# Performance work log

Measured on AMD Instinct MI355X. Metric: run time of the kernel, lower is better.

## Reference

```python
import jax, jax.numpy as jnp
import numpy as np

B, T, D = 2, 1024, 2048      # batch, seq, model dim
E, F, K = 64, 512, 4          # n_experts, expert hidden, top-k
S, HS = 2, 512 * 4            # shared experts, shared hidden = expert_dim * topk


def setup_inputs() -> dict:
    key = jax.random.key(0)
    ks = jax.random.split(key, 9)
    s = 0.02
    f32 = jnp.float32
    return {
        "x": jax.random.normal(ks[0], (B, T, D), f32),
        "router_w": jax.random.normal(ks[1], (D, E), f32) * s,
        "router_bias": jnp.zeros((E,), f32),
        "wg": jax.random.normal(ks[2], (E, D, F), f32) * s,
        "wu": jax.random.normal(ks[3], (E, D, F), f32) * s,
        "wd": jax.random.normal(ks[4], (E, F, D), f32) * s,
        "swg": jax.random.normal(ks[5], (S, D, HS), f32) * s,
        "swu": jax.random.normal(ks[6], (S, D, HS), f32) * s,
        "swd": jax.random.normal(ks[7], (S, HS, D), f32) * s,
    }


def reference(x, router_w, router_bias, wg, wu, wd, swg, swu, swd):
    b, t, d = x.shape
    flat = x.reshape(b * t, d)                      # [N, D]
    n = flat.shape[0]

    # Router: softmax scores, top-k selection on (logits + bias)
    logits = flat @ router_w                         # [N, E]
    scores = jax.nn.softmax(logits, axis=-1)
    _, topk_idx = jax.lax.top_k(logits + router_bias, K)          # [N, K]
    topk_scores = jnp.take_along_axis(scores, topk_idx, axis=-1)  # [N, K]
    topk_scores = topk_scores / topk_scores.sum(axis=-1, keepdims=True)

    # Dense combine weights: w[n, e] = normalized score if expert e selected else 0
    comb = jnp.zeros((n, E), dtype=flat.dtype).at[
        jnp.arange(n)[:, None], topk_idx].set(topk_scores)        # [N, E]

    # Routed experts (SwiGLU), computed densely and masked by combine weights
    g = jax.nn.silu(jnp.einsum('nd,edf->nef', flat, wg))          # [N, E, F]
    u = jnp.einsum('nd,edf->nef', flat, wu)                       # [N, E, F]
    routed = jnp.einsum('ne,nef,efd->nd', comb, g * u, wd)        # [N, D]

    # Shared experts (always active, summed)
    sg = jax.nn.silu(jnp.einsum('nd,sdh->nsh', flat, swg))        # [N, S, HS]
    su = jnp.einsum('nd,sdh->nsh', flat, swu)
    shared = jnp.einsum('nsh,shd->nd', sg * su, swd)              # [N, D]

    return (routed + shared).reshape(b, t, d)
```

## Files before the change

kernel.cpp:

```cpp
#include <hip/hip_runtime.h>
#include <hip/hip_bf16.h>

typedef __bf16 bf16x8 __attribute__((ext_vector_type(8)));
typedef float f32x4 __attribute__((ext_vector_type(4)));
typedef unsigned short u16x4 __attribute__((ext_vector_type(4)));
typedef unsigned short u16x8 __attribute__((ext_vector_type(8)));

#define DEVI __device__ __forceinline__

constexpr int N_TOK = 2048;
constexpr int DIM   = 2048;
constexpr int NEXP  = 64;
constexpr int FDIM  = 512;
constexpr int TOPK  = 4;
constexpr int NSH   = 2;
constexpr int HSH   = 2048;

constexpr int BK = 64, KS = 8;

DEVI unsigned short f2b(float f) {
  union { float fv; unsigned u; } v; v.fv = f;
  unsigned r = v.u + 0x7fffu + ((v.u >> 16) & 1u);
  return (unsigned short)(r >> 16);
}
DEVI float b2f(unsigned short h) {
  union { unsigned u; float f; } v; v.u = ((unsigned)h) << 16;
  return v.f;
}
DEVI void gll16(const void* g, void* l) {
  __builtin_amdgcn_global_load_lds((const __attribute__((address_space(1))) unsigned*)g,
                                   (__attribute__((address_space(3))) unsigned*)l, 16, 0, 0);
}

__global__ void cvt_x_kernel(const float* __restrict__ x, unsigned short* __restrict__ xb) {
  const size_t i = ((size_t)blockIdx.x * 256 + threadIdx.x) * 8;
  const float4 a = *reinterpret_cast<const float4*>(x + i);
  const float4 b = *reinterpret_cast<const float4*>(x + i + 4);
  u16x8 o;
  o[0] = f2b(a.x); o[1] = f2b(a.y); o[2] = f2b(a.z); o[3] = f2b(a.w);
  o[4] = f2b(b.x); o[5] = f2b(b.y); o[6] = f2b(b.z); o[7] = f2b(b.w);
  *reinterpret_cast<u16x8*>(xb + i) = o;
}

__global__ __launch_bounds__(256)
void tr_shared_kernel(const float* __restrict__ swu, const float* __restrict__ swg,
                      const float* __restrict__ swd, unsigned short* __restrict__ swuT,
                      unsigned short* __restrict__ swgT, unsigned short* __restrict__ swdT) {
  __shared__ float Lf[64][68];
  const int tid = threadIdx.x;
  const int r0 = blockIdx.x * 64, c0 = blockIdx.y * 64;
  const int z = blockIdx.z, mat = z >> 1;
  const size_t soff = (size_t)(z & 1) * DIM * HSH;
  const float* in = (mat == 0 ? swu : mat == 1 ? swg : swd) + soff;
  unsigned short* ot = (mat == 0 ? swuT : mat == 1 ? swgT : swdT) + soff;
  #pragma unroll
  for (int j = 0; j < 4; ++j) {
    const int idx = j * 1024 + tid * 4;
    const int row = idx >> 6, col = idx & 63;
    const float4 v = *reinterpret_cast<const float4*>(in + (size_t)(r0 + row) * 2048 + c0 + col);
    *reinterpret_cast<float4*>(&Lf[row][col]) = v;
  }
  __syncthreads();
  #pragma unroll
  for (int j = 0; j < 4; ++j) {
    const int idx = j * 1024 + tid * 4;
    const int orow = idx >> 6, ocol = idx & 63;
    u16x4 o;
    o[0] = f2b(Lf[ocol][orow]);     o[1] = f2b(Lf[ocol + 1][orow]);
    o[2] = f2b(Lf[ocol + 2][orow]); o[3] = f2b(Lf[ocol + 3][orow]);
    *reinterpret_cast<u16x4*>(ot + (size_t)(c0 + orow) * 2048 + r0 + ocol) = o;
  }
}

__global__ __launch_bounds__(256)
void router_kernel(const float* __restrict__ x, const float* __restrict__ rw,
                   const float* __restrict__ rb, int* __restrict__ cnt,
                   int* __restrict__ listTok, float* __restrict__ listW) {
  __shared__ float Lx[8][128];
  const int tid = threadIdx.x;
  const int lane = tid & 63;
  const int wave = tid >> 6;
  const int tokBase = blockIdx.x * 8;

  float acc0 = 0.f, acc1 = 0.f;
  for (int dc = 0; dc < DIM; dc += 128) {
    __syncthreads();
    {
      const int idx = tid * 4;
      const int row = idx >> 7, col = idx & 127;
      *reinterpret_cast<float4*>(&Lx[row][col]) =
          *reinterpret_cast<const float4*>(x + (size_t)(tokBase + row) * DIM + dc + col);
    }
    __syncthreads();
    #pragma unroll 16
    for (int dd = 0; dd < 128; ++dd) {
      const float r = rw[(size_t)(dc + dd) * NEXP + lane];
      acc0 = fmaf(Lx[wave * 2 + 0][dd], r, acc0);
      acc1 = fmaf(Lx[wave * 2 + 1][dd], r, acc1);
    }
  }

  const float bias = rb[lane];
  #pragma unroll
  for (int t = 0; t < 2; ++t) {
    const float v = (t == 0) ? acc0 : acc1;
    const int token = tokBase + wave * 2 + t;
    float m = v;
    #pragma unroll
    for (int o = 32; o > 0; o >>= 1) m = fmaxf(m, __shfl_xor(m, o));
    const float p = expf(v - m);
    float ss = p;
    #pragma unroll
    for (int o = 32; o > 0; o >>= 1) ss += __shfl_xor(ss, o);
    const float score = p / ss;
    float cur = v + bias;
    float wk[TOPK]; int ik[TOPK]; float wsum = 0.f;
    #pragma unroll
    for (int k = 0; k < TOPK; ++k) {
      float tm = cur;
      #pragma unroll
      for (int o = 32; o > 0; o >>= 1) tm = fmaxf(tm, __shfl_xor(tm, o));
      const unsigned long long msk = __ballot(cur == tm);
      const int sel = (int)__builtin_ctzll(msk);
      const float w = __shfl(score, sel);
      wk[k] = w; ik[k] = sel; wsum += w;
      if (lane == sel) cur = -3.4e38f;
    }
    if (lane < TOPK) {
      const int e = ik[lane];
      const float w = wk[lane] / wsum;
      const int slot = atomicAdd(&cnt[e], 1);
      listTok[(size_t)e * N_TOK + slot] = token;
      listW[(size_t)e * N_TOK + slot] = w;
    }
  }
}

__global__ void scan_kernel(const int* __restrict__ cnt, int* __restrict__ off) {
  if (threadIdx.x == 0) {
    int s = 0;
    for (int e = 0; e < NEXP; ++e) { off[e] = s; s += cnt[e]; }
  }
}

template<bool GPASS>
__global__ __launch_bounds__(256, 2)
void up_routed(const unsigned short* __restrict__ xb, const float* __restrict__ W,
               const int* __restrict__ cnt, const int* __restrict__ off,
               const int* __restrict__ listTok, const float* __restrict__ listW,
               unsigned short* __restrict__ H) {
  const int tid = threadIdx.x;
  const int f0 = blockIdx.x * 128;
  const int e  = blockIdx.y;
  const int m0 = blockIdx.z * 128;
  const int c = cnt[e];
  if (m0 >= c) return;
  const int rcnt = min(128, c - m0);
  const int rowbase = off[e] + m0;

  __shared__ __align__(16) unsigned short Al[KS][128][8];
  __shared__ __align__(16) unsigned short Bl[KS][128][8];
  __shared__ int tokS[128];
  __shared__ float wS[128];

  if (tid < 128) {
    tokS[tid] = listTok[(size_t)e * N_TOK + m0 + min(tid, rcnt - 1)];
    wS[tid] = (tid < rcnt) ? listW[(size_t)e * N_TOK + m0 + tid] : 0.f;
  }
  __syncthreads();

  const int wid = tid >> 6, l = tid & 63;
  const int wm = wid >> 1, wn = wid & 1;
  const int lc = l & 15, hi = l >> 4;

  const unsigned short* pa0 = xb + (size_t)tokS[l] * DIM;
  const unsigned short* pa1 = xb + (size_t)tokS[64 + l] * DIM;
  const float* bw = W + (size_t)e * DIM * FDIM + f0;
  const int f4 = tid & 31, k4a = tid >> 5;

  f32x4 acc[4][4];
  #pragma unroll
  for (int i = 0; i < 4; ++i)
    #pragma unroll
    for (int j = 0; j < 4; ++j) acc[i][j] = f32x4{0.f, 0.f, 0.f, 0.f};

  for (int d0 = 0; d0 < DIM; d0 += BK) {
    gll16(pa0 + d0 + (2 * wid) * 8,     &Al[2 * wid][0][0]);
    gll16(pa1 + d0 + (2 * wid) * 8,     &Al[2 * wid][64][0]);
    gll16(pa0 + d0 + (2 * wid + 1) * 8, &Al[2 * wid + 1][0][0]);
    gll16(pa1 + d0 + (2 * wid + 1) * 8, &Al[2 * wid + 1][64][0]);
    f32x4 rB[2][4];
    #pragma unroll
    for (int s2 = 0; s2 < 2; ++s2)
      #pragma unroll
      for (int j = 0; j < 4; ++j)
        rB[s2][j] = *reinterpret_cast<const f32x4*>(
            bw + (size_t)(d0 + k4a * 8 + s2 * 4 + j) * FDIM + f4 * 4);
    #pragma unroll
    for (int cc = 0; cc < 4; ++cc) {
      u16x8 v;
      v[0] = f2b(rB[0][0][cc]); v[1] = f2b(rB[0][1][cc]);
      v[2] = f2b(rB[0][2][cc]); v[3] = f2b(rB[0][3][cc]);
      v[4] = f2b(rB[1][0][cc]); v[5] = f2b(rB[1][1][cc]);
      v[6] = f2b(rB[1][2][cc]); v[7] = f2b(rB[1][3][cc]);
      *reinterpret_cast<u16x8*>(&Bl[k4a][f4 * 4 + cc][0]) = v;
    }
    __syncthreads();
    #pragma unroll
    for (int ks = 0; ks < 2; ++ks) {
      bf16x8 af[4], bq[4];
      #pragma unroll
      for (int i = 0; i < 4; ++i)
        af[i] = *reinterpret_cast<const bf16x8*>(&Al[ks * 4 + hi][wm * 64 + i * 16 + lc][0]);
      #pragma unroll
      for (int i = 0; i < 4; ++i)
        bq[i] = *reinterpret_cast<const bf16x8*>(&Bl[ks * 4 + hi][wn * 64 + i * 16 + lc][0]);
      #pragma unroll
      for (int mi = 0; mi < 4; ++mi)
        #pragma unroll
        for (int ni = 0; ni < 4; ++ni)
          acc[mi][ni] = __builtin_amdgcn_mfma_f32_16x16x32_bf16(af[mi], bq[ni], acc[mi][ni], 0, 0, 0);
    }
    __syncthreads();
  }

  #pragma unroll
  for (int mi = 0; mi < 4; ++mi)
    #pragma unroll
    for (int ni = 0; ni < 4; ++ni)
      #pragma unroll
      for (int r2 = 0; r2 < 4; ++r2) {
        const int row = wm * 64 + mi * 16 + hi * 4 + r2;
        if (row < rcnt) {
          const int col = f0 + wn * 64 + ni * 16 + lc;
          const size_t idx = (size_t)(rowbase + row) * FDIM + col;
          const float v = acc[mi][ni][r2];
          if constexpr (GPASS) {
            const float u = b2f(H[idx]);
            H[idx] = f2b((v / (1.f + __expf(-v))) * u * wS[row]);
          } else {
            H[idx] = f2b(v);
          }
        }
      }
}

__global__ __launch_bounds__(256, 2)
void up_shared(const unsigned short* __restrict__ xb,
               const unsigned short* __restrict__ WuT, const unsigned short* __restrict__ WgT,
               unsigned short* __restrict__ H) {
  const int tid = threadIdx.x;
  const int f0 = blockIdx.x * 64;
  const int s  = blockIdx.y;
  const int m0 = blockIdx.z * 128;

  __shared__ __align__(16) unsigned short Al[KS][128][8];
  __shared__ __align__(16) unsigned short Bu[KS][64][8];
  __shared__ __align__(16) unsigned short Bg[KS][64][8];

  const int wid = tid >> 6, l = tid & 63;
  const int wm = wid >> 1, wn = wid & 1;
  const int lc = l & 15, hi = l >> 4;

  const unsigned short* pa0 = xb + (size_t)(m0 + l) * DIM;
  const unsigned short* pa1 = xb + (size_t)(m0 + 64 + l) * DIM;
  const unsigned short* pbu = WuT + (size_t)s * HSH * DIM + (size_t)(f0 + l) * DIM;
  const unsigned short* pbg = WgT + (size_t)s * HSH * DIM + (size_t)(f0 + l) * DIM;

  f32x4 aU[4][2], aG[4][2];
  #pragma unroll
  for (int i = 0; i < 4; ++i)
    #pragma unroll
    for (int j = 0; j < 2; ++j) { aU[i][j] = f32x4{0.f,0.f,0.f,0.f}; aG[i][j] = f32x4{0.f,0.f,0.f,0.f}; }

  for (int d0 = 0; d0 < DIM; d0 += BK) {
    gll16(pa0 + d0 + (2 * wid) * 8,     &Al[2 * wid][0][0]);
    gll16(pa1 + d0 + (2 * wid) * 8,     &Al[2 * wid][64][0]);
    gll16(pa0 + d0 + (2 * wid + 1) * 8, &Al[2 * wid + 1][0][0]);
    gll16(pa1 + d0 + (2 * wid + 1) * 8, &Al[2 * wid + 1][64][0]);
    gll16(pbu + d0 + (2 * wid) * 8,     &Bu[2 * wid][0][0]);
    gll16(pbu + d0 + (2 * wid + 1) * 8, &Bu[2 * wid + 1][0][0]);
    gll16(pbg + d0 + (2 * wid) * 8,     &Bg[2 * wid][0][0]);
    gll16(pbg + d0 + (2 * wid + 1) * 8, &Bg[2 * wid + 1][0][0]);
    __syncthreads();
    #pragma unroll
    for (int ks = 0; ks < 2; ++ks) {
      bf16x8 af[4], bu[2], bg[2];
      #pragma unroll
      for (int i = 0; i < 4; ++i)
        af[i] = *reinterpret_cast<const bf16x8*>(&Al[ks * 4 + hi][wm * 64 + i * 16 + lc][0]);
      #pragma unroll
      for (int i = 0; i < 2; ++i) {
        bu[i] = *reinterpret_cast<const bf16x8*>(&Bu[ks * 4 + hi][wn * 32 + i * 16 + lc][0]);
        bg[i] = *reinterpret_cast<const bf16x8*>(&Bg[ks * 4 + hi][wn * 32 + i * 16 + lc][0]);
      }
      #pragma unroll
      for (int mi = 0; mi < 4; ++mi)
        #pragma unroll
        for (int ni = 0; ni < 2; ++ni) {
          aU[mi][ni] = __builtin_amdgcn_mfma_f32_16x16x32_bf16(af[mi], bu[ni], aU[mi][ni], 0, 0, 0);
          aG[mi][ni] = __builtin_amdgcn_mfma_f32_16x16x32_bf16(af[mi], bg[ni], aG[mi][ni], 0, 0, 0);
        }
    }
    __syncthreads();
  }

  #pragma unroll
  for (int mi = 0; mi < 4; ++mi)
    #pragma unroll
    for (int ni = 0; ni < 2; ++ni)
      #pragma unroll
      for (int r2 = 0; r2 < 4; ++r2) {
        const int row = wm * 64 + mi * 16 + hi * 4 + r2;
        const int col = f0 + wn * 32 + ni * 16 + lc;
        const float g = aG[mi][ni][r2], u = aU[mi][ni][r2];
        const float h = (g / (1.f + __expf(-g))) * u;
        H[((size_t)s * N_TOK + m0 + row) * HSH + col] = f2b(h);
      }
}

__global__ __launch_bounds__(256, 2)
void down_all(const unsigned short* __restrict__ Hr, const unsigned short* __restrict__ Hs,
              const float* __restrict__ wd, const unsigned short* __restrict__ swdT,
              const int* __restrict__ cnt, const int* __restrict__ off,
              const int* __restrict__ listTok, float* __restrict__ out) {
  const int tid = threadIdx.x;
  const int x0 = blockIdx.x * 128;
  const int y  = blockIdx.y;
  const int m0 = blockIdx.z * 128;
  const bool routed = y < NEXP;

  __shared__ __align__(16) unsigned short Al[KS][128][8];
  __shared__ __align__(16) unsigned short Bl[KS][128][8];
  __shared__ int tokS[128];

  const int wid = tid >> 6, l = tid & 63;
  const int wm = wid >> 1, wn = wid & 1;
  const int lc = l & 15, hi = l >> 4;

  int rcnt = 128, Kd;
  const unsigned short *pa0, *pa1, *pb0 = nullptr, *pb1 = nullptr;
  const float* bw = nullptr;

  if (routed) {
    const int c = cnt[y];
    if (m0 >= c) return;
    rcnt = min(128, c - m0);
    const int rowbase = off[y] + m0;
    Kd = FDIM;
    if (tid < 128) tokS[tid] = listTok[(size_t)y * N_TOK + m0 + min(tid, rcnt - 1)];
    pa0 = Hr + (size_t)(rowbase + min(l, rcnt - 1)) * FDIM;
    pa1 = Hr + (size_t)(rowbase + min(64 + l, rcnt - 1)) * FDIM;
    bw = wd + (size_t)y * FDIM * DIM + x0;
  } else {
    const int s = y - NEXP;
    Kd = HSH;
    if (tid < 128) tokS[tid] = m0 + tid;
    pa0 = Hs + ((size_t)s * N_TOK + m0 + l) * HSH;
    pa1 = Hs + ((size_t)s * N_TOK + m0 + 64 + l) * HSH;
    pb0 = swdT + (size_t)s * HSH * DIM + (size_t)(x0 + l) * HSH;
    pb1 = swdT + (size_t)s * HSH * DIM + (size_t)(x0 + 64 + l) * HSH;
  }

  const int f4 = tid & 31, k4a = tid >> 5;

  f32x4 acc[4][4];
  #pragma unroll
  for (int i = 0; i < 4; ++i)
    #pragma unroll
    for (int j = 0; j < 4; ++j) acc[i][j] = f32x4{0.f, 0.f, 0.f, 0.f};

  for (int d0 = 0; d0 < Kd; d0 += BK) {
    gll16(pa0 + d0 + (2 * wid) * 8,     &Al[2 * wid][0][0]);
    gll16(pa1 + d0 + (2 * wid) * 8,     &Al[2 * wid][64][0]);
    gll16(pa0 + d0 + (2 * wid + 1) * 8, &Al[2 * wid + 1][0][0]);
    gll16(pa1 + d0 + (2 * wid + 1) * 8, &Al[2 * wid + 1][64][0]);
    if (routed) {
      f32x4 rB[2][4];
      #pragma unroll
      for (int s2 = 0; s2 < 2; ++s2)
        #pragma unroll
        for (int j = 0; j < 4; ++j)
          rB[s2][j] = *reinterpret_cast<const f32x4*>(
              bw + (size_t)(d0 + k4a * 8 + s2 * 4 + j) * DIM + f4 * 4);
      #pragma unroll
      for (int cc = 0; cc < 4; ++cc) {
        u16x8 v;
        v[0] = f2b(rB[0][0][cc]); v[1] = f2b(rB[0][1][cc]);
        v[2] = f2b(rB[0][2][cc]); v[3] = f2b(rB[0][3][cc]);
        v[4] = f2b(rB[1][0][cc]); v[5] = f2b(rB[1][1][cc]);
        v[6] = f2b(rB[1][2][cc]); v[7] = f2b(rB[1][3][cc]);
        *reinterpret_cast<u16x8*>(&Bl[k4a][f4 * 4 + cc][0]) = v;
      }
    } else {
      gll16(pb0 + d0 + (2 * wid) * 8,     &Bl[2 * wid][0][0]);
      gll16(pb1 + d0 + (2 * wid) * 8,     &Bl[2 * wid][64][0]);
      gll16(pb0 + d0 + (2 * wid + 1) * 8, &Bl[2 * wid + 1][0][0]);
      gll16(pb1 + d0 + (2 * wid + 1) * 8, &Bl[2 * wid + 1][64][0]);
    }
    __syncthreads();
    #pragma unroll
    for (int ks = 0; ks < 2; ++ks) {
      bf16x8 af[4], bq[4];
      #pragma unroll
      for (int i = 0; i < 4; ++i)
        af[i] = *reinterpret_cast<const bf16x8*>(&Al[ks * 4 + hi][wm * 64 + i * 16 + lc][0]);
      #pragma unroll
      for (int i = 0; i < 4; ++i)
        bq[i] = *reinterpret_cast<const bf16x8*>(&Bl[ks * 4 + hi][wn * 64 + i * 16 + lc][0]);
      #pragma unroll
      for (int mi = 0; mi < 4; ++mi)
        #pragma unroll
        for (int ni = 0; ni < 4; ++ni)
          acc[mi][ni] = __builtin_amdgcn_mfma_f32_16x16x32_bf16(af[mi], bq[ni], acc[mi][ni], 0, 0, 0);
    }
    __syncthreads();
  }

  #pragma unroll
  for (int mi = 0; mi < 4; ++mi)
    #pragma unroll
    for (int ni = 0; ni < 4; ++ni)
      #pragma unroll
      for (int r2 = 0; r2 < 4; ++r2) {
        const int row = wm * 64 + mi * 16 + hi * 4 + r2;
        if (row < rcnt) {
          const int col = x0 + wn * 64 + ni * 16 + lc;
          atomicAdd(&out[(size_t)tokS[row] * DIM + col], acc[mi][ni][r2]);
        }
      }
}

extern "C" void kernel_launch(void* const* d_in, const int* in_sizes, int n_in,
                              void* d_out, int out_size, void* d_ws, size_t ws_size,
                              hipStream_t stream) {
  const float* x   = (const float*)d_in[0];
  const float* rw  = (const float*)d_in[1];
  const float* rb  = (const float*)d_in[2];
  const float* wg  = (const float*)d_in[3];
  const float* wu  = (const float*)d_in[4];
  const float* wd  = (const float*)d_in[5];
  const float* swg = (const float*)d_in[6];
  const float* swu = (const float*)d_in[7];
  const float* swd = (const float*)d_in[8];
  float* out = (float*)d_out;
  char* ws = (char*)d_ws;

  int* cnt = (int*)ws;
  int* off = (int*)(ws + 256);
  int* listTok = (int*)(ws + 4096);
  float* listW = (float*)(ws + 4096 + 512 * 1024);
  unsigned short* xb   = (unsigned short*)(ws + (size_t) 2 * 1024 * 1024);
  unsigned short* Hr   = (unsigned short*)(ws + (size_t)10 * 1024 * 1024);
  unsigned short* Hs   = (unsigned short*)(ws + (size_t)18 * 1024 * 1024);
  unsigned short* swuT = (unsigned short*)(ws + (size_t)34 * 1024 * 1024);
  unsigned short* swgT = (unsigned short*)(ws + (size_t)50 * 1024 * 1024);
  unsigned short* swdT = (unsigned short*)(ws + (size_t)66 * 1024 * 1024);

  hipMemsetAsync(cnt, 0, NEXP * sizeof(int), stream);
  hipMemsetAsync(out, 0, (size_t)N_TOK * DIM * sizeof(float), stream);
  cvt_x_kernel<<<(N_TOK * DIM) / (256 * 8), 256, 0, stream>>>(x, xb);
  tr_shared_kernel<<<dim3(32, 32, 6), 256, 0, stream>>>(swu, swg, swd, swuT, swgT, swdT);
  router_kernel<<<N_TOK / 8, 256, 0, stream>>>(x, rw, rb, cnt, listTok, listW);
  scan_kernel<<<1, 64, 0, stream>>>(cnt, off);

  up_routed<false><<<dim3(FDIM / 128, NEXP, 16), 256, 0, stream>>>(
      xb, wu, cnt, off, listTok, listW, Hr);
  up_routed<true><<<dim3(FDIM / 128, NEXP, 16), 256, 0, stream>>>(
      xb, wg, cnt, off, listTok, listW, Hr);
  up_shared<<<dim3(HSH / 64, NSH, N_TOK / 128), 256, 0, stream>>>(
      xb, swuT, swgT, Hs);
  down_all<<<dim3(DIM / 128, NEXP + NSH, 16), 256, 0, stream>>>(
      Hr, Hs, wd, swdT, cnt, off, listTok, out);
}
```

Measured before the change: 687.6 us.

## Fuse routed gate/up GEMMs, double-buffer pipelines, replace atomic scatter with combine

The separate up and gate passes over routed experts become one kernel that computes both accumulators and applies SwiGLU in the epilogue, so the gathered activations are read once. All GEMM kernels move to double-buffered LDS with explicit vmcnt waits, so the next tile's loads overlap the current MFMAs. The down projection splits into a shared kernel that writes out directly (the memset goes away) and a routed kernel that writes bf16 partials. A combine kernel then sums each token's four partials, replacing float atomics. This adds a partials buffer, an extra launch and bf16 rounding of the partials.

```diff
diff --git a/kernel.cpp b/kernel.cpp
--- a/kernel.cpp
+++ b/kernel.cpp
@@ -17,6 +17,12 @@
 constexpr int HSH   = 2048;
 
 constexpr int BK = 64, KS = 8;
+
+#define WAIT_VM0 asm volatile("s_waitcnt vmcnt(0)" ::: "memory")
+#define WAIT_VM8 asm volatile("s_waitcnt vmcnt(8)" ::: "memory")
+#define WAIT_LG0 asm volatile("s_waitcnt lgkmcnt(0)" ::: "memory")
+#define SBAR __builtin_amdgcn_s_barrier()
+#define SCHED0 __builtin_amdgcn_sched_barrier(0)
 
 DEVI unsigned short f2b(float f) {
   union { float fv; unsigned u; } v; v.fv = f;
@@ -75,7 +81,8 @@
 __global__ __launch_bounds__(256)
 void router_kernel(const float* __restrict__ x, const float* __restrict__ rw,
                    const float* __restrict__ rb, int* __restrict__ cnt,
-                   int* __restrict__ listTok, float* __restrict__ listW) {
+                   int* __restrict__ listTok, float* __restrict__ listW,
+                   int* __restrict__ tokEP) {
   __shared__ float Lx[8][128];
   const int tid = threadIdx.x;
   const int lane = tid & 63;
@@ -132,6 +139,7 @@
       const int slot = atomicAdd(&cnt[e], 1);
       listTok[(size_t)e * N_TOK + slot] = token;
       listW[(size_t)e * N_TOK + slot] = w;
+      tokEP[token * TOPK + lane] = (e << 16) | slot;
     }
   }
 }
@@ -143,14 +151,15 @@
   }
 }
 
-template<bool GPASS>
 __global__ __launch_bounds__(256, 2)
-void up_routed(const unsigned short* __restrict__ xb, const float* __restrict__ W,
+void up_routed(const unsigned short* __restrict__ xb,
+               const float* __restrict__ Wu, const float* __restrict__ Wg,
                const int* __restrict__ cnt, const int* __restrict__ off,
                const int* __restrict__ listTok, const float* __restrict__ listW,
                unsigned short* __restrict__ H) {
+  constexpr int NT = DIM / BK;
   const int tid = threadIdx.x;
-  const int f0 = blockIdx.x * 128;
+  const int f0 = blockIdx.x * 64;
   const int e  = blockIdx.y;
   const int m0 = blockIdx.z * 128;
   const int c = cnt[e];
@@ -158,44 +167,316 @@
   const int rcnt = min(128, c - m0);
   const int rowbase = off[e] + m0;
 
-  __shared__ __align__(16) unsigned short Al[KS][128][8];
-  __shared__ __align__(16) unsigned short Bl[KS][128][8];
-  __shared__ int tokS[128];
-  __shared__ float wS[128];
-
-  if (tid < 128) {
-    tokS[tid] = listTok[(size_t)e * N_TOK + m0 + min(tid, rcnt - 1)];
-    wS[tid] = (tid < rcnt) ? listW[(size_t)e * N_TOK + m0 + tid] : 0.f;
-  }
+  __shared__ __align__(16) unsigned short Al[2][KS][128][8];
+  __shared__ __align__(16) unsigned short BuL[2][KS][64][8];
+  __shared__ __align__(16) unsigned short BgL[2][KS][64][8];
+  __shared__ float wSs[128];
+
+  if (tid < 128) wSs[tid] = (tid < rcnt) ? listW[(size_t)e * N_TOK + m0 + tid] : 0.f;
   __syncthreads();
 
   const int wid = tid >> 6, l = tid & 63;
   const int wm = wid >> 1, wn = wid & 1;
   const int lc = l & 15, hi = l >> 4;
 
-  const unsigned short* pa0 = xb + (size_t)tokS[l] * DIM;
-  const unsigned short* pa1 = xb + (size_t)tokS[64 + l] * DIM;
-  const float* bw = W + (size_t)e * DIM * FDIM + f0;
-  const int f4 = tid & 31, k4a = tid >> 5;
-
-  f32x4 acc[4][4];
+  const int t0 = listTok[(size_t)e * N_TOK + m0 + min(l, rcnt - 1)];
+  const int t1 = listTok[(size_t)e * N_TOK + m0 + min(64 + l, rcnt - 1)];
+  const unsigned short* pa0 = xb + (size_t)t0 * DIM;
+  const unsigned short* pa1 = xb + (size_t)t1 * DIM;
+  const float* wub = Wu + (size_t)e * DIM * FDIM + f0;
+  const float* wgb = Wg + (size_t)e * DIM * FDIM + f0;
+
+  const int q = tid & 31, p = tid >> 5;
+  const int c4 = (q & 15) * 4, kh = q >> 4;
+
+  f32x4 rBu[4], rBg[4];
+  auto loadB = [&](int g) {
+    const int d0 = g * BK;
+    #pragma unroll
+    for (int j = 0; j < 4; ++j)
+      rBu[j] = *reinterpret_cast<const f32x4*>(wub + (size_t)(d0 + p * 8 + kh * 4 + j) * FDIM + c4);
+    #pragma unroll
+    for (int j = 0; j < 4; ++j)
+      rBg[j] = *reinterpret_cast<const f32x4*>(wgb + (size_t)(d0 + p * 8 + kh * 4 + j) * FDIM + c4);
+  };
+  auto stageA = [&](int g, int b) {
+    const int d0 = g * BK;
+    gll16(pa0 + d0 + (2 * wid) * 8,     &Al[b][2 * wid][0][0]);
+    gll16(pa1 + d0 + (2 * wid) * 8,     &Al[b][2 * wid][64][0]);
+    gll16(pa0 + d0 + (2 * wid + 1) * 8, &Al[b][2 * wid + 1][0][0]);
+    gll16(pa1 + d0 + (2 * wid + 1) * 8, &Al[b][2 * wid + 1][64][0]);
+  };
+  auto writeB = [&](int b) {
+    #pragma unroll
+    for (int cc = 0; cc < 4; ++cc) {
+      u16x4 vu, vg;
+      #pragma unroll
+      for (int j = 0; j < 4; ++j) { vu[j] = f2b(rBu[j][cc]); vg[j] = f2b(rBg[j][cc]); }
+      *reinterpret_cast<u16x4*>(&BuL[b][p][c4 + cc][kh * 4]) = vu;
+      *reinterpret_cast<u16x4*>(&BgL[b][p][c4 + cc][kh * 4]) = vg;
+    }
+  };
+
+  f32x4 aU[4][2], aG[4][2];
   #pragma unroll
   for (int i = 0; i < 4; ++i)
     #pragma unroll
-    for (int j = 0; j < 4; ++j) acc[i][j] = f32x4{0.f, 0.f, 0.f, 0.f};
-
-  for (int d0 = 0; d0 < DIM; d0 += BK) {
-    gll16(pa0 + d0 + (2 * wid) * 8,     &Al[2 * wid][0][0]);
-    gll16(pa1 + d0 + (2 * wid) * 8,     &Al[2 * wid][64][0]);
-    gll16(pa0 + d0 + (2 * wid + 1) * 8, &Al[2 * wid + 1][0][0]);
-    gll16(pa1 + d0 + (2 * wid + 1) * 8, &Al[2 * wid + 1][64][0]);
-    f32x4 rB[2][4];
+    for (int j = 0; j < 2; ++j) { aU[i][j] = f32x4{0,0,0,0}; aG[i][j] = f32x4{0,0,0,0}; }
+
+  loadB(0);
+  stageA(0, 0);
+  SCHED0;
+  writeB(0);
+  loadB(1);
+  WAIT_VM8; WAIT_LG0; SBAR;
+
+  for (int g = 0; g < NT; ++g) {
+    const int b = g & 1;
+    if (g + 1 < NT) {
+      stageA(g + 1, b ^ 1);
+      SCHED0;
+      writeB(b ^ 1);
+      if (g + 2 < NT) loadB(g + 2);
+    }
+    #pragma unroll
+    for (int ks = 0; ks < 2; ++ks) {
+      bf16x8 af[4], bu[2], bg[2];
+      #pragma unroll
+      for (int i = 0; i < 4; ++i)
+        af[i] = *reinterpret_cast<const bf16x8*>(&Al[b][ks * 4 + hi][wm * 64 + i * 16 + lc][0]);
+      #pragma unroll
+      for (int i = 0; i < 2; ++i) {
+        bu[i] = *reinterpret_cast<const bf16x8*>(&BuL[b][ks * 4 + hi][wn * 32 + i * 16 + lc][0]);
+        bg[i] = *reinterpret_cast<const bf16x8*>(&BgL[b][ks * 4 + hi][wn * 32 + i * 16 + lc][0]);
+      }
+      #pragma unroll
+      for (int mi = 0; mi < 4; ++mi)
+        #pragma unroll
+        for (int ni = 0; ni < 2; ++ni) {
+          aU[mi][ni] = __builtin_amdgcn_mfma_f32_16x16x32_bf16(af[mi], bu[ni], aU[mi][ni], 0, 0, 0);
+          aG[mi][ni] = __builtin_amdgcn_mfma_f32_16x16x32_bf16(af[mi], bg[ni], aG[mi][ni], 0, 0, 0);
+        }
+    }
+    if (g + 1 < NT) {
+      if (g + 2 < NT) { WAIT_VM8; } else { WAIT_VM0; }
+      WAIT_LG0; SBAR;
+    }
+  }
+
+  #pragma unroll
+  for (int mi = 0; mi < 4; ++mi)
+    #pragma unroll
+    for (int ni = 0; ni < 2; ++ni)
+      #pragma unroll
+      for (int r2 = 0; r2 < 4; ++r2) {
+        const int row = wm * 64 + mi * 16 + hi * 4 + r2;
+        if (row < rcnt) {
+          const int col = f0 + wn * 32 + ni * 16 + lc;
+          const float g = aG[mi][ni][r2], u = aU[mi][ni][r2];
+          const float h = (g / (1.f + __expf(-g))) * u * wSs[row];
+          H[(size_t)(rowbase + row) * FDIM + col] = f2b(h);
+        }
+      }
+}
+
+__global__ __launch_bounds__(256, 2)
+void up_shared(const unsigned short* __restrict__ xb,
+               const unsigned short* __restrict__ WuT, const unsigned short* __restrict__ WgT,
+               unsigned short* __restrict__ H) {
+  constexpr int NT = DIM / BK;
+  const int tid = threadIdx.x;
+  const int f0 = blockIdx.x * 64;
+  const int s  = blockIdx.y;
+  const int m0 = blockIdx.z * 128;
+
+  __shared__ __align__(16) unsigned short Al[2][KS][128][8];
+  __shared__ __align__(16) unsigned short Bu[2][KS][64][8];
+  __shared__ __align__(16) unsigned short Bg[2][KS][64][8];
+
+  const int wid = tid >> 6, l = tid & 63;
+  const int wm = wid >> 1, wn = wid & 1;
+  const int lc = l & 15, hi = l >> 4;
+
+  const unsigned short* pa0 = xb + (size_t)(m0 + l) * DIM;
+  const unsigned short* pa1 = xb + (size_t)(m0 + 64 + l) * DIM;
+  const unsigned short* pbu = WuT + (size_t)s * HSH * DIM + (size_t)(f0 + l) * DIM;
+  const unsigned short* pbg = WgT + (size_t)s * HSH * DIM + (size_t)(f0 + l) * DIM;
+
+  auto stage = [&](int g, int b) {
+    const int d0 = g * BK;
+    gll16(pa0 + d0 + (2 * wid) * 8,     &Al[b][2 * wid][0][0]);
+    gll16(pa1 + d0 + (2 * wid) * 8,     &Al[b][2 * wid][64][0]);
+    gll16(pa0 + d0 + (2 * wid + 1) * 8, &Al[b][2 * wid + 1][0][0]);
+    gll16(pa1 + d0 + (2 * wid + 1) * 8, &Al[b][2 * wid + 1][64][0]);
+    gll16(pbu + d0 + (2 * wid) * 8,     &Bu[b][2 * wid][0][0]);
+    gll16(pbu + d0 + (2 * wid + 1) * 8, &Bu[b][2 * wid + 1][0][0]);
+    gll16(pbg + d0 + (2 * wid) * 8,     &Bg[b][2 * wid][0][0]);
+    gll16(pbg + d0 + (2 * wid + 1) * 8, &Bg[b][2 * wid + 1][0][0]);
+  };
+
+  f32x4 aU[4][2], aG[4][2];
+  #pragma unroll
+  for (int i = 0; i < 4; ++i)
+    #pragma unroll
+    for (int j = 0; j < 2; ++j) { aU[i][j] = f32x4{0,0,0,0}; aG[i][j] = f32x4{0,0,0,0}; }
+
+  stage(0, 0);
+  WAIT_VM0; SBAR;
+
+  for (int g = 0; g < NT; ++g) {
+    const int b = g & 1;
+    if (g + 1 < NT) stage(g + 1, b ^ 1);
+    #pragma unroll
+    for (int ks = 0; ks < 2; ++ks) {
+      bf16x8 af[4], bu[2], bg[2];
+      #pragma unroll
+      for (int i = 0; i < 4; ++i)
+        af[i] = *reinterpret_cast<const bf16x8*>(&Al[b][ks * 4 + hi][wm * 64 + i * 16 + lc][0]);
+      #pragma unroll
+      for (int i = 0; i < 2; ++i) {
+        bu[i] = *reinterpret_cast<const bf16x8*>(&Bu[b][ks * 4 + hi][wn * 32 + i * 16 + lc][0]);
+        bg[i] = *reinterpret_cast<const bf16x8*>(&Bg[b][ks * 4 + hi][wn * 32 + i * 16 + lc][0]);
+      }
+      #pragma unroll
+      for (int mi = 0; mi < 4; ++mi)
+        #pragma unroll
+        for (int ni = 0; ni < 2; ++ni) {
+          aU[mi][ni] = __builtin_amdgcn_mfma_f32_16x16x32_bf16(af[mi], bu[ni], aU[mi][ni], 0, 0, 0);
+          aG[mi][ni] = __builtin_amdgcn_mfma_f32_16x16x32_bf16(af[mi], bg[ni], aG[mi][ni], 0, 0, 0);
+        }
+    }
+    if (g + 1 < NT) { WAIT_VM0; SBAR; }
+  }
+
+  #pragma unroll
+  for (int mi = 0; mi < 4; ++mi)
+    #pragma unroll
+    for (int ni = 0; ni < 2; ++ni)
+      #pragma unroll
+      for (int r2 = 0; r2 < 4; ++r2) {
+        const int row = wm * 64 + mi * 16 + hi * 4 + r2;
+        const int col = f0 + wn * 32 + ni * 16 + lc;
+        const float g = aG[mi][ni][r2], u = aU[mi][ni][r2];
+        H[((size_t)s * N_TOK + m0 + row) * HSH + col] = f2b((g / (1.f + __expf(-g))) * u);
+      }
+}
+
+__global__ __launch_bounds__(256, 3)
+void down_shared(const unsigned short* __restrict__ Hs, const unsigned short* __restrict__ swdT,
+                 float* __restrict__ out) {
+  constexpr int NT = 2 * HSH / BK;
+  const int tid = threadIdx.x;
+  const int x0 = blockIdx.x * 128;
+  const int m0 = blockIdx.z * 64;
+
+  __shared__ __align__(16) unsigned short Al[2][KS][64][8];
+  __shared__ __align__(16) unsigned short Bl[2][KS][128][8];
+
+  const int wid = tid >> 6, l = tid & 63;
+  const int wm = wid >> 1, wn = wid & 1;
+  const int lc = l & 15, hi = l >> 4;
+
+  auto stage = [&](int g, int b) {
+    const int seg = g >> 5;
+    const int d0 = (g & 31) * BK;
+    const unsigned short* sA = Hs + ((size_t)seg * N_TOK + m0 + l) * HSH + d0;
+    const unsigned short* b0 = swdT + (size_t)seg * HSH * DIM + (size_t)(x0 + l) * HSH + d0;
+    const unsigned short* b1 = b0 + (size_t)64 * HSH;
+    gll16(sA + (2 * wid) * 8,     &Al[b][2 * wid][0][0]);
+    gll16(sA + (2 * wid + 1) * 8, &Al[b][2 * wid + 1][0][0]);
+    gll16(b0 + (2 * wid) * 8,     &Bl[b][2 * wid][0][0]);
+    gll16(b1 + (2 * wid) * 8,     &Bl[b][2 * wid][64][0]);
+    gll16(b0 + (2 * wid + 1) * 8, &Bl[b][2 * wid + 1][0][0]);
+    gll16(b1 + (2 * wid + 1) * 8, &Bl[b][2 * wid + 1][64][0]);
+  };
+
+  f32x4 acc[2][4];
+  #pragma unroll
+  for (int i = 0; i < 2; ++i)
+    #pragma unroll
+    for (int j = 0; j < 4; ++j) acc[i][j] = f32x4{0,0,0,0};
+
+  stage(0, 0);
+  WAIT_VM0; SBAR;
+
+  for (int g = 0; g < NT; ++g) {
+    const int b = g & 1;
+    if (g + 1 < NT) stage(g + 1, b ^ 1);
+    #pragma unroll
+    for (int ks = 0; ks < 2; ++ks) {
+      bf16x8 af[2], bq[4];
+      #pragma unroll
+      for (int i = 0; i < 2; ++i)
+        af[i] = *reinterpret_cast<const bf16x8*>(&Al[b][ks * 4 + hi][wm * 32 + i * 16 + lc][0]);
+      #pragma unroll
+      for (int i = 0; i < 4; ++i)
+        bq[i] = *reinterpret_cast<const bf16x8*>(&Bl[b][ks * 4 + hi][wn * 64 + i * 16 + lc][0]);
+      #pragma unroll
+      for (int mi = 0; mi < 2; ++mi)
+        #pragma unroll
+        for (int ni = 0; ni < 4; ++ni)
+          acc[mi][ni] = __builtin_amdgcn_mfma_f32_16x16x32_bf16(af[mi], bq[ni], acc[mi][ni], 0, 0, 0);
+    }
+    if (g + 1 < NT) { WAIT_VM0; SBAR; }
+  }
+
+  #pragma unroll
+  for (int mi = 0; mi < 2; ++mi)
+    #pragma unroll
+    for (int ni = 0; ni < 4; ++ni)
+      #pragma unroll
+      for (int r2 = 0; r2 < 4; ++r2) {
+        const int row = wm * 32 + mi * 16 + hi * 4 + r2;
+        const int col = x0 + wn * 64 + ni * 16 + lc;
+        out[(size_t)(m0 + row) * DIM + col] = acc[mi][ni][r2];
+      }
+}
+
+__global__ __launch_bounds__(256, 2)
+void down_routed(const unsigned short* __restrict__ Hr, const float* __restrict__ wd,
+                 const int* __restrict__ cnt, const int* __restrict__ off,
+                 unsigned short* __restrict__ P) {
+  constexpr int NT = FDIM / BK;
+  const int tid = threadIdx.x;
+  const int x0 = blockIdx.x * 128;
+  const int e  = blockIdx.y;
+  const int m0 = blockIdx.z * 128;
+  const int c = cnt[e];
+  if (m0 >= c) return;
+  const int rcnt = min(128, c - m0);
+  const int rowbase = off[e] + m0;
+
+  __shared__ __align__(16) unsigned short Al[2][KS][128][8];
+  __shared__ __align__(16) unsigned short Bl[2][KS][128][8];
+
+  const int wid = tid >> 6, l = tid & 63;
+  const int wm = wid >> 1, wn = wid & 1;
+  const int lc = l & 15, hi = l >> 4;
+
+  const unsigned short* pa0 = Hr + (size_t)(rowbase + min(l, rcnt - 1)) * FDIM;
+  const unsigned short* pa1 = Hr + (size_t)(rowbase + min(64 + l, rcnt - 1)) * FDIM;
+  const float* bw = wd + (size_t)e * FDIM * DIM + x0;
+
+  const int f4 = tid & 31, p = tid >> 5;
+  const int c4 = f4 * 4;
+
+  f32x4 rB[2][4];
+  auto loadB = [&](int g) {
+    const int d0 = g * BK;
     #pragma unroll
     for (int s2 = 0; s2 < 2; ++s2)
       #pragma unroll
       for (int j = 0; j < 4; ++j)
-        rB[s2][j] = *reinterpret_cast<const f32x4*>(
-            bw + (size_t)(d0 + k4a * 8 + s2 * 4 + j) * FDIM + f4 * 4);
+        rB[s2][j] = *reinterpret_cast<const f32x4*>(bw + (size_t)(d0 + p * 8 + s2 * 4 + j) * DIM + c4);
+  };
+  auto stageA = [&](int g, int b) {
+    const int d0 = g * BK;
+    gll16(pa0 + d0 + (2 * wid) * 8,     &Al[b][2 * wid][0][0]);
+    gll16(pa1 + d0 + (2 * wid) * 8,     &Al[b][2 * wid][64][0]);
+    gll16(pa0 + d0 + (2 * wid + 1) * 8, &Al[b][2 * wid + 1][0][0]);
+    gll16(pa1 + d0 + (2 * wid + 1) * 8, &Al[b][2 * wid + 1][64][0]);
+  };
+  auto writeB = [&](int b) {
     #pragma unroll
     for (int cc = 0; cc < 4; ++cc) {
       u16x8 v;
@@ -203,218 +484,50 @@
       v[2] = f2b(rB[0][2][cc]); v[3] = f2b(rB[0][3][cc]);
       v[4] = f2b(rB[1][0][cc]); v[5] = f2b(rB[1][1][cc]);
       v[6] = f2b(rB[1][2][cc]); v[7] = f2b(rB[1][3][cc]);
-      *reinterpret_cast<u16x8*>(&Bl[k4a][f4 * 4 + cc][0]) = v;
-    }
-    __syncthreads();
+      *reinterpret_cast<u16x8*>(&Bl[b][p][c4 + cc][0]) = v;
+    }
+  };
+
+  f32x4 acc[4][4];
+  #pragma unroll
+  for (int i = 0; i < 4; ++i)
+    #pragma unroll
+    for (int j = 0; j < 4; ++j) acc[i][j] = f32x4{0,0,0,0};
+
+  loadB(0);
+  stageA(0, 0);
+  SCHED0;
+  writeB(0);
+  loadB(1);
+  WAIT_VM8; WAIT_LG0; SBAR;
+
+  for (int g = 0; g < NT; ++g) {
+    const int b = g & 1;
+    if (g + 1 < NT) {
+      stageA(g + 1, b ^ 1);
+      SCHED0;
+      writeB(b ^ 1);
+      if (g + 2 < NT) loadB(g + 2);
+    }
     #pragma unroll
     for (int ks = 0; ks < 2; ++ks) {
       bf16x8 af[4], bq[4];
       #pragma unroll
       for (int i = 0; i < 4; ++i)
-        af[i] = *reinterpret_cast<const bf16x8*>(&Al[ks * 4 + hi][wm * 64 + i * 16 + lc][0]);
+        af[i] = *reinterpret_cast<const bf16x8*>(&Al[b][ks * 4 + hi][wm * 64 + i * 16 + lc][0]);
       #pragma unroll
       for (int i = 0; i < 4; ++i)
-        bq[i] = *reinterpret_cast<const bf16x8*>(&Bl[ks * 4 + hi][wn * 64 + i * 16 + lc][0]);
+        bq[i] = *reinterpret_cast<const bf16x8*>(&Bl[b][ks * 4 + hi][wn * 64 + i * 16 + lc][0]);
       #pragma unroll
       for (int mi = 0; mi < 4; ++mi)
         #pragma unroll
         for (int ni = 0; ni < 4; ++ni)
           acc[mi][ni] = __builtin_amdgcn_mfma_f32_16x16x32_bf16(af[mi], bq[ni], acc[mi][ni], 0, 0, 0);
     }
-    __syncthreads();
-  }
-
-  #pragma unroll
-  for (int mi = 0; mi < 4; ++mi)
-    #pragma unroll
-    for (int ni = 0; ni < 4; ++ni)
-      #pragma unroll
-      for (int r2 = 0; r2 < 4; ++r2) {
-        const int row = wm * 64 + mi * 16 + hi * 4 + r2;
-        if (row < rcnt) {
-          const int col = f0 + wn * 64 + ni * 16 + lc;
-          const size_t idx = (size_t)(rowbase + row) * FDIM + col;
-          const float v = acc[mi][ni][r2];
-          if constexpr (GPASS) {
-            const float u = b2f(H[idx]);
-            H[idx] = f2b((v / (1.f + __expf(-v))) * u * wS[row]);
-          } else {
-            H[idx] = f2b(v);
-          }
-        }
-      }
-}
-
-__global__ __launch_bounds__(256, 2)
-void up_shared(const unsigned short* __restrict__ xb,
-               const unsigned short* __restrict__ WuT, const unsigned short* __restrict__ WgT,
-               unsigned short* __restrict__ H) {
-  const int tid = threadIdx.x;
-  const int f0 = blockIdx.x * 64;
-  const int s  = blockIdx.y;
-  const int m0 = blockIdx.z * 128;
-
-  __shared__ __align__(16) unsigned short Al[KS][128][8];
-  __shared__ __align__(16) unsigned short Bu[KS][64][8];
-  __shared__ __align__(16) unsigned short Bg[KS][64][8];
-
-  const int wid = tid >> 6, l = tid & 63;
-  const int wm = wid >> 1, wn = wid & 1;
-  const int lc = l & 15, hi = l >> 4;
-
-  const unsigned short* pa0 = xb + (size_t)(m0 + l) * DIM;
-  const unsigned short* pa1 = xb + (size_t)(m0 + 64 + l) * DIM;
-  const unsigned short* pbu = WuT + (size_t)s * HSH * DIM + (size_t)(f0 + l) * DIM;
-  const unsigned short* pbg = WgT + (size_t)s * HSH * DIM + (size_t)(f0 + l) * DIM;
-
-  f32x4 aU[4][2], aG[4][2];
-  #pragma unroll
-  for (int i = 0; i < 4; ++i)
-    #pragma unroll
-    for (int j = 0; j < 2; ++j) { aU[i][j] = f32x4{0.f,0.f,0.f,0.f}; aG[i][j] = f32x4{0.f,0.f,0.f,0.f}; }
-
-  for (int d0 = 0; d0 < DIM; d0 += BK) {
-    gll16(pa0 + d0 + (2 * wid) * 8,     &Al[2 * wid][0][0]);
-    gll16(pa1 + d0 + (2 * wid) * 8,     &Al[2 * wid][64][0]);
-    gll16(pa0 + d0 + (2 * wid + 1) * 8, &Al[2 * wid + 1][0][0]);
-    gll16(pa1 + d0 + (2 * wid + 1) * 8, &Al[2 * wid + 1][64][0]);
-    gll16(pbu + d0 + (2 * wid) * 8,     &Bu[2 * wid][0][0]);
-    gll16(pbu + d0 + (2 * wid + 1) * 8, &Bu[2 * wid + 1][0][0]);
-    gll16(pbg + d0 + (2 * wid) * 8,     &Bg[2 * wid][0][0]);
-    gll16(pbg + d0 + (2 * wid + 1) * 8, &Bg[2 * wid + 1][0][0]);
-    __syncthreads();
-    #pragma unroll
-    for (int ks = 0; ks < 2; ++ks) {
-      bf16x8 af[4], bu[2], bg[2];
-      #pragma unroll
-      for (int i = 0; i < 4; ++i)
-        af[i] = *reinterpret_cast<const bf16x8*>(&Al[ks * 4 + hi][wm * 64 + i * 16 + lc][0]);
-      #pragma unroll
-      for (int i = 0; i < 2; ++i) {
-        bu[i] = *reinterpret_cast<const bf16x8*>(&Bu[ks * 4 + hi][wn * 32 + i * 16 + lc][0]);
-        bg[i] = *reinterpret_cast<const bf16x8*>(&Bg[ks * 4 + hi][wn * 32 + i * 16 + lc][0]);
-      }
-      #pragma unroll
-      for (int mi = 0; mi < 4; ++mi)
-        #pragma unroll
-        for (int ni = 0; ni < 2; ++ni) {
-          aU[mi][ni] = __builtin_amdgcn_mfma_f32_16x16x32_bf16(af[mi], bu[ni], aU[mi][ni], 0, 0, 0);
-          aG[mi][ni] = __builtin_amdgcn_mfma_f32_16x16x32_bf16(af[mi], bg[ni], aG[mi][ni], 0, 0, 0);
-        }
-    }
-    __syncthreads();
-  }
-
-  #pragma unroll
-  for (int mi = 0; mi < 4; ++mi)
-    #pragma unroll
-    for (int ni = 0; ni < 2; ++ni)
-      #pragma unroll
-      for (int r2 = 0; r2 < 4; ++r2) {
-        const int row = wm * 64 + mi * 16 + hi * 4 + r2;
-        const int col = f0 + wn * 32 + ni * 16 + lc;
-        const float g = aG[mi][ni][r2], u = aU[mi][ni][r2];
-        const float h = (g / (1.f + __expf(-g))) * u;
-        H[((size_t)s * N_TOK + m0 + row) * HSH + col] = f2b(h);
-      }
-}
-
-__global__ __launch_bounds__(256, 2)
-void down_all(const unsigned short* __restrict__ Hr, const unsigned short* __restrict__ Hs,
-              const float* __restrict__ wd, const unsigned short* __restrict__ swdT,
-              const int* __restrict__ cnt, const int* __restrict__ off,
-              const int* __restrict__ listTok, float* __restrict__ out) {
-  const int tid = threadIdx.x;
-  const int x0 = blockIdx.x * 128;
-  const int y  = blockIdx.y;
-  const int m0 = blockIdx.z * 128;
-  const bool routed = y < NEXP;
-
-  __shared__ __align__(16) unsigned short Al[KS][128][8];
-  __shared__ __align__(16) unsigned short Bl[KS][128][8];
-  __shared__ int tokS[128];
-
-  const int wid = tid >> 6, l = tid & 63;
-  const int wm = wid >> 1, wn = wid & 1;
-  const int lc = l & 15, hi = l >> 4;
-
-  int rcnt = 128, Kd;
-  const unsigned short *pa0, *pa1, *pb0 = nullptr, *pb1 = nullptr;
-  const float* bw = nullptr;
-
-  if (routed) {
-    const int c = cnt[y];
-    if (m0 >= c) return;
-    rcnt = min(128, c - m0);
-    const int rowbase = off[y] + m0;
-    Kd = FDIM;
-    if (tid < 128) tokS[tid] = listTok[(size_t)y * N_TOK + m0 + min(tid, rcnt - 1)];
-    pa0 = Hr + (size_t)(rowbase + min(l, rcnt - 1)) * FDIM;
-    pa1 = Hr + (size_t)(rowbase + min(64 + l, rcnt - 1)) * FDIM;
-    bw = wd + (size_t)y * FDIM * DIM + x0;
-  } else {
-    const int s = y - NEXP;
-    Kd = HSH;
-    if (tid < 128) tokS[tid] = m0 + tid;
-    pa0 = Hs + ((size_t)s * N_TOK + m0 + l) * HSH;
-    pa1 = Hs + ((size_t)s * N_TOK + m0 + 64 + l) * HSH;
-    pb0 = swdT + (size_t)s * HSH * DIM + (size_t)(x0 + l) * HSH;
-    pb1 = swdT + (size_t)s * HSH * DIM + (size_t)(x0 + 64 + l) * HSH;
-  }
-
-  const int f4 = tid & 31, k4a = tid >> 5;
-
-  f32x4 acc[4][4];
-  #pragma unroll
-  for (int i = 0; i < 4; ++i)
-    #pragma unroll
-    for (int j = 0; j < 4; ++j) acc[i][j] = f32x4{0.f, 0.f, 0.f, 0.f};
-
-  for (int d0 = 0; d0 < Kd; d0 += BK) {
-    gll16(pa0 + d0 + (2 * wid) * 8,     &Al[2 * wid][0][0]);
-    gll16(pa1 + d0 + (2 * wid) * 8,     &Al[2 * wid][64][0]);
-    gll16(pa0 + d0 + (2 * wid + 1) * 8, &Al[2 * wid + 1][0][0]);
-    gll16(pa1 + d0 + (2 * wid + 1) * 8, &Al[2 * wid + 1][64][0]);
-    if (routed) {
-      f32x4 rB[2][4];
-      #pragma unroll
-      for (int s2 = 0; s2 < 2; ++s2)
-        #pragma unroll
-        for (int j = 0; j < 4; ++j)
-          rB[s2][j] = *reinterpret_cast<const f32x4*>(
-              bw + (size_t)(d0 + k4a * 8 + s2 * 4 + j) * DIM + f4 * 4);
-      #pragma unroll
-      for (int cc = 0; cc < 4; ++cc) {
-        u16x8 v;
-        v[0] = f2b(rB[0][0][cc]); v[1] = f2b(rB[0][1][cc]);
-        v[2] = f2b(rB[0][2][cc]); v[3] = f2b(rB[0][3][cc]);
-        v[4] = f2b(rB[1][0][cc]); v[5] = f2b(rB[1][1][cc]);
-        v[6] = f2b(rB[1][2][cc]); v[7] = f2b(rB[1][3][cc]);
-        *reinterpret_cast<u16x8*>(&Bl[k4a][f4 * 4 + cc][0]) = v;
-      }
-    } else {
-      gll16(pb0 + d0 + (2 * wid) * 8,     &Bl[2 * wid][0][0]);
-      gll16(pb1 + d0 + (2 * wid) * 8,     &Bl[2 * wid][64][0]);
-      gll16(pb0 + d0 + (2 * wid + 1) * 8, &Bl[2 * wid + 1][0][0]);
-      gll16(pb1 + d0 + (2 * wid + 1) * 8, &Bl[2 * wid + 1][64][0]);
-    }
-    __syncthreads();
-    #pragma unroll
-    for (int ks = 0; ks < 2; ++ks) {
-      bf16x8 af[4], bq[4];
-      #pragma unroll
-      for (int i = 0; i < 4; ++i)
-        af[i] = *reinterpret_cast<const bf16x8*>(&Al[ks * 4 + hi][wm * 64 + i * 16 + lc][0]);
-      #pragma unroll
-      for (int i = 0; i < 4; ++i)
-        bq[i] = *reinterpret_cast<const bf16x8*>(&Bl[ks * 4 + hi][wn * 64 + i * 16 + lc][0]);
-      #pragma unroll
-      for (int mi = 0; mi < 4; ++mi)
-        #pragma unroll
-        for (int ni = 0; ni < 4; ++ni)
-          acc[mi][ni] = __builtin_amdgcn_mfma_f32_16x16x32_bf16(af[mi], bq[ni], acc[mi][ni], 0, 0, 0);
-    }
-    __syncthreads();
+    if (g + 1 < NT) {
+      if (g + 2 < NT) { WAIT_VM8; } else { WAIT_VM0; }
+      WAIT_LG0; SBAR;
+    }
   }
 
   #pragma unroll
@@ -426,9 +539,34 @@
         const int row = wm * 64 + mi * 16 + hi * 4 + r2;
         if (row < rcnt) {
           const int col = x0 + wn * 64 + ni * 16 + lc;
-          atomicAdd(&out[(size_t)tokS[row] * DIM + col], acc[mi][ni][r2]);
+          P[(size_t)(rowbase + row) * DIM + col] = f2b(acc[mi][ni][r2]);
         }
       }
+}
+
+__global__ __launch_bounds__(256)
+void combine_kernel(const int* __restrict__ tokEP, const int* __restrict__ off,
+                    const unsigned short* __restrict__ P, float* __restrict__ out) {
+  const int n = blockIdx.x;
+  const int tid = threadIdx.x;
+  int rows[4];
+  #pragma unroll
+  for (int k = 0; k < TOPK; ++k) {
+    const int ep = tokEP[n * TOPK + k];
+    rows[k] = off[ep >> 16] + (ep & 0xffff);
+  }
+  const int cc = tid * 8;
+  float* po = out + (size_t)n * DIM + cc;
+  float4 o0 = *reinterpret_cast<const float4*>(po);
+  float4 o1 = *reinterpret_cast<const float4*>(po + 4);
+  #pragma unroll
+  for (int k = 0; k < TOPK; ++k) {
+    const u16x8 v = *reinterpret_cast<const u16x8*>(P + (size_t)rows[k] * DIM + cc);
+    o0.x += b2f(v[0]); o0.y += b2f(v[1]); o0.z += b2f(v[2]); o0.w += b2f(v[3]);
+    o1.x += b2f(v[4]); o1.y += b2f(v[5]); o1.z += b2f(v[6]); o1.w += b2f(v[7]);
+  }
+  *reinterpret_cast<float4*>(po) = o0;
+  *reinterpret_cast<float4*>(po + 4) = o1;
 }
 
 extern "C" void kernel_launch(void* const* d_in, const int* in_sizes, int n_in,
@@ -448,28 +586,30 @@
 
   int* cnt = (int*)ws;
   int* off = (int*)(ws + 256);
-  int* listTok = (int*)(ws + 4096);
-  float* listW = (float*)(ws + 4096 + 512 * 1024);
+  int* tokEP = (int*)(ws + 4096);
+  int* listTok = (int*)(ws + 64 * 1024);
+  float* listW = (float*)(ws + 576 * 1024);
   unsigned short* xb   = (unsigned short*)(ws + (size_t) 2 * 1024 * 1024);
   unsigned short* Hr   = (unsigned short*)(ws + (size_t)10 * 1024 * 1024);
   unsigned short* Hs   = (unsigned short*)(ws + (size_t)18 * 1024 * 1024);
   unsigned short* swuT = (unsigned short*)(ws + (size_t)34 * 1024 * 1024);
   unsigned short* swgT = (unsigned short*)(ws + (size_t)50 * 1024 * 1024);
   unsigned short* swdT = (unsigned short*)(ws + (size_t)66 * 1024 * 1024);
+  unsigned short* P    = (unsigned short*)(ws + (size_t)82 * 1024 * 1024);
 
   hipMemsetAsync(cnt, 0, NEXP * sizeof(int), stream);
-  hipMemsetAsync(out, 0, (size_t)N_TOK * DIM * sizeof(float), stream);
   cvt_x_kernel<<<(N_TOK * DIM) / (256 * 8), 256, 0, stream>>>(x, xb);
   tr_shared_kernel<<<dim3(32, 32, 6), 256, 0, stream>>>(swu, swg, swd, swuT, swgT, swdT);
-  router_kernel<<<N_TOK / 8, 256, 0, stream>>>(x, rw, rb, cnt, listTok, listW);
+  router_kernel<<<N_TOK / 8, 256, 0, stream>>>(x, rw, rb, cnt, listTok, listW, tokEP);
   scan_kernel<<<1, 64, 0, stream>>>(cnt, off);
 
-  up_routed<false><<<dim3(FDIM / 128, NEXP, 16), 256, 0, stream>>>(
-      xb, wu, cnt, off, listTok, listW, Hr);
-  up_routed<true><<<dim3(FDIM / 128, NEXP, 16), 256, 0, stream>>>(
-      xb, wg, cnt, off, listTok, listW, Hr);
+  up_routed<<<dim3(FDIM / 64, NEXP, 16), 256, 0, stream>>>(
+      xb, wu, wg, cnt, off, listTok, listW, Hr);
   up_shared<<<dim3(HSH / 64, NSH, N_TOK / 128), 256, 0, stream>>>(
       xb, swuT, swgT, Hs);
-  down_all<<<dim3(DIM / 128, NEXP + NSH, 16), 256, 0, stream>>>(
-      Hr, Hs, wd, swdT, cnt, off, listTok, out);
-}
+  down_shared<<<dim3(DIM / 128, 1, N_TOK / 64), 256, 0, stream>>>(
+      Hs, swdT, out);
+  down_routed<<<dim3(DIM / 128, NEXP, 16), 256, 0, stream>>>(
+      Hr, wd, cnt, off, P);
+  combine_kernel<<<N_TOK, 256, 0, stream>>>(tokEP, off, P, out);
+}
```

Measured after the change: 723.1 us. 1.05x slower.
